# Performance work log

Measured on AMD Instinct MI355X. Metric: run time of the kernel, lower is better.

Reference implementation:

```python
import jax, jax.numpy as jnp
import numpy as np

IMG = 224          # mask height/width, hardcoded in the module
OUT = 256          # Linear(224*224 -> 256)
BOX = 20           # half-width of the square mask around the farthest joint


def setup_inputs() -> dict:
    key = jax.random.key(0)
    k1, k2, k3, k4 = jax.random.split(key, 4)
    B, J, T = 256, 25, 64
    rgbfuture = jax.random.normal(k1, (B, OUT), dtype=jnp.float32)
    # normalized joint coords kept in [0.1, 0.9] so pixel_x in [22, 201] (original
    # code has no x-clamping and would hit numpy negative-slice wraparound otherwise)
    skeleton_future = 0.1 + 0.8 * jax.random.uniform(k2, (B, J, T, 3), dtype=jnp.float32)
    W = jax.random.normal(k3, (OUT, IMG * IMG), dtype=jnp.float32) / np.sqrt(IMG * IMG)
    b = jax.random.normal(k4, (OUT,), dtype=jnp.float32) * 0.01
    return {"rgbfuture": rgbfuture, "skeleton_future": skeleton_future, "W": W, "b": b}


def reference(rgbfuture, skeleton_future, W, b):
    B, J, T, _ = skeleton_future.shape
    mid = J // 2

    # distance of every joint trajectory to the middle joint, per frame: [B, J, T]
    diff = skeleton_future - skeleton_future[:, mid:mid + 1]
    dist = jnp.linalg.norm(diff, axis=-1)
    t_max = jnp.argmax(dist, axis=-1)                       # [B, J]

    # farthest-frame coordinates per joint: [B, J, 3]
    pts = jnp.take_along_axis(skeleton_future, t_max[:, :, None, None], axis=2)[:, :, 0, :]
    px = (pts[..., 0] * IMG).astype(jnp.int32)              # int() truncation == floor (positive)
    py = (pts[..., 1] * IMG).astype(jnp.int32)

    rows = jnp.arange(IMG)
    # x-range: [px-20, px+20) (inputs guarantee in-frame)
    xm = (rows >= (px - BOX)[..., None]) & (rows < (px + BOX)[..., None])   # [B, J, IMG]
    # y-range with the module's explicit edge handling
    y_lo = jnp.where(py < BOX, 0, py - BOX)
    y_hi = jnp.where(py > IMG - BOX, IMG, py + BOX)
    ym = (rows >= y_lo[..., None]) & (rows < y_hi[..., None])               # [B, J, IMG]

    keep = jnp.arange(J) != mid                              # middle joint is skipped
    box = xm[:, :, :, None] & ym[:, :, None, :] & keep[None, :, None, None]  # [B, J, IMG, IMG]
    mask = jnp.any(box, axis=1).astype(rgbfuture.dtype)      # torch.max over joints == union

    merged = mask.reshape(B, IMG * IMG) @ W.T + b            # [B, 256]
    return rgbfuture * merged
```

## Files before the change

### kernel.cpp

```cpp
#include <hip/hip_runtime.h>
#include <hip/hip_bf16.h>
#include <stdint.h>

#define IMG   224
#define OUTD  256
#define BATCH 256
#define JD    25
#define TD    64
#define MIDJ  12
#define BOXR  20

typedef float vfloat4 __attribute__((ext_vector_type(4)));

#define OFF_EV   25804800u
#define OFF_EVC  27901952u
#define OFF_PART 27910144u


__global__ void KA(const float* __restrict__ W, __hip_bfloat16* __restrict__ P,
                   const float* __restrict__ skel, uint32_t* __restrict__ evlist,
                   uint32_t* __restrict__ evcnt) {
    const int id  = blockIdx.x;
    const int tid = threadIdx.x;

    __shared__ float lds[64][225];
    __shared__ float carry[8][64];
    __shared__ int s_px[JD], s_ylo[JD], s_yhi[JD];
    __shared__ uint32_t s_n[IMG];

    if (id < 896) {
        const int xcd = id & 7;
        const int g   = id >> 3;
        const int oc  = g & 3;
        const int xi  = g >> 2;
        const int x   = xcd * 28 + xi;
        const int o0  = oc * 64;

        #pragma unroll
        for (int it = 0; it < 7; ++it) {
            const int k = it * 512 + tid;
            const int r = k / 56;
            const int c = k - r * 56;
            const vfloat4 v = __builtin_nontemporal_load(
                (const vfloat4*)&W[(size_t)(o0 + r) * (IMG * IMG) + (size_t)x * IMG + c * 4]);
            lds[r][c * 4 + 0] = v.x;
            lds[r][c * 4 + 1] = v.y;
            lds[r][c * 4 + 2] = v.z;
            lds[r][c * 4 + 3] = v.w;
        }
        __syncthreads();

        const int ol  = tid & 63;
        const int seg = tid >> 6;
        const int y0  = seg * 28;

        float ssum = 0.0f;
        #pragma unroll
        for (int i = 0; i < 28; ++i) ssum += lds[ol][y0 + i];
        carry[seg][ol] = ssum;
        __syncthreads();

        float s = 0.0f;
        for (int s2 = 0; s2 < seg; ++s2) s += carry[s2][ol];

        __hip_bfloat16* p = P + ((size_t)x * 225) * 256 + o0 + ol;
        if (seg == 0) p[0] = __float2bfloat16(0.0f);
        #pragma unroll
        for (int i = 0; i < 28; ++i) {
            s += lds[ol][y0 + i];
            p[(size_t)(y0 + i + 1) * 256] = __float2bfloat16(s);
        }
        return;
    }

    const int b = id - 896;
    const int wave = tid >> 6;
    const int t = tid & 63;

    const float* sb = skel + (size_t)b * JD * TD * 3;
    const float mx = sb[(MIDJ * TD + t) * 3 + 0];
    const float my = sb[(MIDJ * TD + t) * 3 + 1];
    const float mz = sb[(MIDJ * TD + t) * 3 + 2];

    for (int j = wave; j < JD; j += 8) {
        const float ax = sb[(j * TD + t) * 3 + 0];
        const float ay = sb[(j * TD + t) * 3 + 1];
        const float az = sb[(j * TD + t) * 3 + 2];
        const float dx = ax - mx, dy = ay - my, dz = az - mz;
        const float d2 = __fadd_rn(__fadd_rn(__fmul_rn(dx, dx), __fmul_rn(dy, dy)),
                                   __fmul_rn(dz, dz));
        float bd = sqrtf(d2);
        int   bi = t;
        #pragma unroll
        for (int off = 1; off < 64; off <<= 1) {
            const float od = __shfl_xor(bd, off);
            const int   oi = __shfl_xor(bi, off);
            if (od > bd || (od == bd && oi < bi)) { bd = od; bi = oi; }
        }
        if (t == 0) {
            const float ptx = sb[(j * TD + bi) * 3 + 0];
            const float pty = sb[(j * TD + bi) * 3 + 1];
            const int px = (int)(ptx * 224.0f);
            const int py = (int)(pty * 224.0f);
            s_px[j]  = px;
            s_ylo[j] = (py < BOXR) ? 0 : (py - BOXR);
            s_yhi[j] = (py > IMG - BOXR) ? IMG : (py + BOXR);
        }
    }
    __syncthreads();

    const int x = tid;
    unsigned long long m0 = 0, m1 = 0, m2 = 0, m3 = 0;
    uint32_t n = 0;
    if (x < IMG) {
        for (int j = 0; j < JD; ++j) {
            if (j == MIDJ) continue;
            const int px = s_px[j];
            if (x >= px - BOXR && x < px + BOXR) {
                const int lo = s_ylo[j], hi = s_yhi[j];
                auto setw = [&](unsigned long long& mw, int wbase) {
                    int l = lo - wbase; int h = hi - wbase;
                    l = l < 0 ? 0 : l; h = h > 64 ? 64 : h;
                    if (l < h) {
                        unsigned long long msk =
                            (h - l == 64) ? ~0ull : ((((1ull << (h - l)) - 1ull)) << l);
                        mw |= msk;
                    }
                };
                setw(m0, 0); setw(m1, 64); setw(m2, 128); setw(m3, 192);
            }
        }
        const unsigned long long e0 = m0 & ~(m0 << 1);
        const unsigned long long e1 = m1 & ~((m1 << 1) | (m0 >> 63));
        const unsigned long long e2 = m2 & ~((m2 << 1) | (m1 >> 63));
        const unsigned long long e3 = m3 & ~((m3 << 1) | (m2 >> 63));
        n = (uint32_t)(__popcll(e0) + __popcll(e1) + __popcll(e2) + __popcll(e3));
        s_n[x] = n;
    }
    __syncthreads();
    if (x >= IMG) return;

    const int sl = x / 28;
    const int xl = x - sl * 28;
    uint32_t off = 0;
    for (int i = sl * 28; i < x; ++i) off += s_n[i];
    if (xl == 27) evcnt[(size_t)b * 8 + sl] = off + n;

    uint32_t* evs = evlist + ((size_t)b * 8 + sl) * 256 + off;
    int k = 0, start = -1;
    auto scanw = [&](unsigned long long bits, int wbase) {
        int pos = 0;
        while (pos < 64) {
            if (start < 0) {
                const unsigned long long tt = bits >> pos;
                if (!tt) return;
                pos += __builtin_ctzll(tt);
                start = wbase + pos;
            } else {
                const unsigned long long tt = (~bits) >> pos;
                if (!tt) return;
                pos += __builtin_ctzll(tt);
                evs[k] = (uint32_t)xl | ((uint32_t)start << 5)
                                      | ((uint32_t)(wbase + pos) << 13);
                ++k; start = -1;
            }
        }
    };
    scanw(m0, 0); scanw(m1, 64); scanw(m2, 128); scanw(m3, 192);
    if (start >= 0) { evs[k] = (uint32_t)xl | ((uint32_t)start << 5) | (224u << 13); }
}

__global__ void k_accum(const uint32_t* __restrict__ evlist,
                        const uint32_t* __restrict__ evcnt,
                        const uint32_t* __restrict__ P32,
                        float* __restrict__ part) {
    const int bs  = blockIdx.x;
    const int s   = bs & 7;
    const int tid = threadIdx.x;
    const int x0  = s * 28;

    __shared__ uint32_t slist[256];

    const uint32_t cntv = evcnt[bs];
    slist[tid]       = evlist[(size_t)bs * 256 + tid];
    slist[128 + tid] = evlist[(size_t)bs * 256 + 128 + tid];
    __syncthreads();

    const int total = (int)cntv;
    const uint32_t* Pbase = P32 + (size_t)x0 * (225 * 128) + tid;

    float a0 = 0.f, a1 = 0.f, b0 = 0.f, b1 = 0.f;
    float c0 = 0.f, c1 = 0.f, d0 = 0.f, d1 = 0.f;
    int i = 0;
    for (; i + 4 <= total; i += 4) {
        const uint32_t e0 = slist[i], e1 = slist[i + 1];
        const uint32_t e2 = slist[i + 2], e3 = slist[i + 3];
        const uint32_t* p0 = Pbase + (size_t)(e0 & 31u) * (225 * 128);
        const uint32_t* p1 = Pbase + (size_t)(e1 & 31u) * (225 * 128);
        const uint32_t* p2 = Pbase + (size_t)(e2 & 31u) * (225 * 128);
        const uint32_t* p3 = Pbase + (size_t)(e3 & 31u) * (225 * 128);
        const uint32_t va0 = p0[(size_t)((e0 >> 5) & 255u) * 128];
        const uint32_t vc0 = p0[(size_t)((e0 >> 13) & 255u) * 128];
        const uint32_t va1 = p1[(size_t)((e1 >> 5) & 255u) * 128];
        const uint32_t vc1 = p1[(size_t)((e1 >> 13) & 255u) * 128];
        const uint32_t va2 = p2[(size_t)((e2 >> 5) & 255u) * 128];
        const uint32_t vc2 = p2[(size_t)((e2 >> 13) & 255u) * 128];
        const uint32_t va3 = p3[(size_t)((e3 >> 5) & 255u) * 128];
        const uint32_t vc3 = p3[(size_t)((e3 >> 13) & 255u) * 128];
        a0 += __uint_as_float(vc0 << 16) - __uint_as_float(va0 << 16);
        a1 += __uint_as_float(vc0 & 0xffff0000u) - __uint_as_float(va0 & 0xffff0000u);
        b0 += __uint_as_float(vc1 << 16) - __uint_as_float(va1 << 16);
        b1 += __uint_as_float(vc1 & 0xffff0000u) - __uint_as_float(va1 & 0xffff0000u);
        c0 += __uint_as_float(vc2 << 16) - __uint_as_float(va2 << 16);
        c1 += __uint_as_float(vc2 & 0xffff0000u) - __uint_as_float(va2 & 0xffff0000u);
        d0 += __uint_as_float(vc3 << 16) - __uint_as_float(va3 << 16);
        d1 += __uint_as_float(vc3 & 0xffff0000u) - __uint_as_float(va3 & 0xffff0000u);
    }
    for (; i < total; ++i) {
        const uint32_t e0 = slist[i];
        const uint32_t* p0 = Pbase + (size_t)(e0 & 31u) * (225 * 128);
        const uint32_t va0 = p0[(size_t)((e0 >> 5) & 255u) * 128];
        const uint32_t vc0 = p0[(size_t)((e0 >> 13) & 255u) * 128];
        a0 += __uint_as_float(vc0 << 16) - __uint_as_float(va0 << 16);
        a1 += __uint_as_float(vc0 & 0xffff0000u) - __uint_as_float(va0 & 0xffff0000u);
    }

    float* pp = part + ((size_t)bs * 256) + (size_t)tid * 2;
    pp[0] = (a0 + b0) + (c0 + d0);
    pp[1] = (a1 + b1) + (c1 + d1);
}

__global__ void k_final(const float* __restrict__ rgb, const float* __restrict__ bias,
                        const float* __restrict__ part, float* __restrict__ out) {
    const int idx = blockIdx.x * 256 + threadIdx.x;
    const int b = idx >> 8, o = idx & 255;
    float m = bias[o];
    #pragma unroll
    for (int s = 0; s < 8; ++s) m += part[(((size_t)b * 8 + s) * 256) + o];
    out[idx] = rgb[idx] * m;
}

extern "C" void kernel_launch(void* const* d_in, const int* in_sizes, int n_in,
                              void* d_out, int out_size, void* d_ws, size_t ws_size,
                              hipStream_t stream) {
    const float* rgb  = (const float*)d_in[0];
    const float* skel = (const float*)d_in[1];
    const float* W    = (const float*)d_in[2];
    const float* bias = (const float*)d_in[3];
    float* out = (float*)d_out;

    uint8_t* ws = (uint8_t*)d_ws;
    __hip_bfloat16* P = (__hip_bfloat16*)(ws);
    uint32_t* evlist = (uint32_t*)(ws + OFF_EV);
    uint32_t* evcnt  = (uint32_t*)(ws + OFF_EVC);
    float* part = (float*)(ws + OFF_PART);

    KA<<<dim3(1152), dim3(512), 0, stream>>>(W, P, skel, evlist, evcnt);
    k_accum<<<dim3(BATCH * 8), dim3(128), 0, stream>>>(evlist, evcnt, (const uint32_t*)P, part);
    k_final<<<dim3(BATCH), dim3(256), 0, stream>>>(rgb, bias, part, out);
}
```

Baseline: 41.76 us.

## Split x-range into 16 slices, widen gather unroll, cache prefix row in registers

```diff
diff --git a/kernel.cpp b/kernel.cpp
--- a/kernel.cpp
+++ b/kernel.cpp
@@ -9,12 +9,14 @@
 #define TD    64
 #define MIDJ  12
 #define BOXR  20
+#define NSL   16
+#define SLW   14
 
 typedef float vfloat4 __attribute__((ext_vector_type(4)));
 
 #define OFF_EV   25804800u
-#define OFF_EVC  27901952u
-#define OFF_PART 27910144u
+#define OFF_EVC  29999104u
+#define OFF_PART 30015488u
 
 
 __global__ void KA(const float* __restrict__ W, __hip_bfloat16* __restrict__ P,
@@ -30,23 +32,25 @@
 
     if (id < 896) {
         const int xcd = id & 7;
-        const int g   = id >> 3;
-        const int oc  = g & 3;
-        const int xi  = g >> 2;
-        const int x   = xcd * 28 + xi;
+        const int r   = id >> 3;
+        const int oc  = r & 3;
+        const int q   = r >> 2;
+        const int xi  = q % 14;
+        const int hi8 = q / 14;
+        const int x   = (hi8 * 8 + xcd) * SLW + xi;
         const int o0  = oc * 64;
 
         #pragma unroll
         for (int it = 0; it < 7; ++it) {
             const int k = it * 512 + tid;
-            const int r = k / 56;
-            const int c = k - r * 56;
+            const int rr = k / 56;
+            const int c  = k - rr * 56;
             const vfloat4 v = __builtin_nontemporal_load(
-                (const vfloat4*)&W[(size_t)(o0 + r) * (IMG * IMG) + (size_t)x * IMG + c * 4]);
-            lds[r][c * 4 + 0] = v.x;
-            lds[r][c * 4 + 1] = v.y;
-            lds[r][c * 4 + 2] = v.z;
-            lds[r][c * 4 + 3] = v.w;
+                (const vfloat4*)&W[(size_t)(o0 + rr) * (IMG * IMG) + (size_t)x * IMG + c * 4]);
+            lds[rr][c * 4 + 0] = v.x;
+            lds[rr][c * 4 + 1] = v.y;
+            lds[rr][c * 4 + 2] = v.z;
+            lds[rr][c * 4 + 3] = v.w;
         }
         __syncthreads();
 
@@ -54,9 +58,13 @@
         const int seg = tid >> 6;
         const int y0  = seg * 28;
 
+        float rv[28];
+        #pragma unroll
+        for (int i = 0; i < 28; ++i) rv[i] = lds[ol][y0 + i];
+
         float ssum = 0.0f;
         #pragma unroll
-        for (int i = 0; i < 28; ++i) ssum += lds[ol][y0 + i];
+        for (int i = 0; i < 28; ++i) ssum += rv[i];
         carry[seg][ol] = ssum;
         __syncthreads();
 
@@ -67,7 +75,7 @@
         if (seg == 0) p[0] = __float2bfloat16(0.0f);
         #pragma unroll
         for (int i = 0; i < 28; ++i) {
-            s += lds[ol][y0 + i];
+            s += rv[i];
             p[(size_t)(y0 + i + 1) * 256] = __float2bfloat16(s);
         }
         return;
@@ -140,13 +148,13 @@
     __syncthreads();
     if (x >= IMG) return;
 
-    const int sl = x / 28;
-    const int xl = x - sl * 28;
+    const int sl = x / SLW;
+    const int xl = x - sl * SLW;
     uint32_t off = 0;
-    for (int i = sl * 28; i < x; ++i) off += s_n[i];
-    if (xl == 27) evcnt[(size_t)b * 8 + sl] = off + n;
-
-    uint32_t* evs = evlist + ((size_t)b * 8 + sl) * 256 + off;
+    for (int i = sl * SLW; i < x; ++i) off += s_n[i];
+    if (xl == SLW - 1) evcnt[(size_t)b * NSL + sl] = off + n;
+
+    uint32_t* evs = evlist + ((size_t)b * NSL + sl) * 256 + off;
     int k = 0, start = -1;
     auto scanw = [&](unsigned long long bits, int wbase) {
         int pos = 0;
@@ -175,9 +183,9 @@
                         const uint32_t* __restrict__ P32,
                         float* __restrict__ part) {
     const int bs  = blockIdx.x;
-    const int s   = bs & 7;
+    const int s   = bs & (NSL - 1);
     const int tid = threadIdx.x;
-    const int x0  = s * 28;
+    const int x0  = s * SLW;
 
     __shared__ uint32_t slist[256];
 
@@ -189,45 +197,42 @@
     const int total = (int)cntv;
     const uint32_t* Pbase = P32 + (size_t)x0 * (225 * 128) + tid;
 
-    float a0 = 0.f, a1 = 0.f, b0 = 0.f, b1 = 0.f;
-    float c0 = 0.f, c1 = 0.f, d0 = 0.f, d1 = 0.f;
+    float aLo[8] = {0.f,0.f,0.f,0.f,0.f,0.f,0.f,0.f};
+    float aHi[8] = {0.f,0.f,0.f,0.f,0.f,0.f,0.f,0.f};
     int i = 0;
-    for (; i + 4 <= total; i += 4) {
-        const uint32_t e0 = slist[i], e1 = slist[i + 1];
-        const uint32_t e2 = slist[i + 2], e3 = slist[i + 3];
-        const uint32_t* p0 = Pbase + (size_t)(e0 & 31u) * (225 * 128);
-        const uint32_t* p1 = Pbase + (size_t)(e1 & 31u) * (225 * 128);
-        const uint32_t* p2 = Pbase + (size_t)(e2 & 31u) * (225 * 128);
-        const uint32_t* p3 = Pbase + (size_t)(e3 & 31u) * (225 * 128);
-        const uint32_t va0 = p0[(size_t)((e0 >> 5) & 255u) * 128];
-        const uint32_t vc0 = p0[(size_t)((e0 >> 13) & 255u) * 128];
-        const uint32_t va1 = p1[(size_t)((e1 >> 5) & 255u) * 128];
-        const uint32_t vc1 = p1[(size_t)((e1 >> 13) & 255u) * 128];
-        const uint32_t va2 = p2[(size_t)((e2 >> 5) & 255u) * 128];
-        const uint32_t vc2 = p2[(size_t)((e2 >> 13) & 255u) * 128];
-        const uint32_t va3 = p3[(size_t)((e3 >> 5) & 255u) * 128];
-        const uint32_t vc3 = p3[(size_t)((e3 >> 13) & 255u) * 128];
-        a0 += __uint_as_float(vc0 << 16) - __uint_as_float(va0 << 16);
-        a1 += __uint_as_float(vc0 & 0xffff0000u) - __uint_as_float(va0 & 0xffff0000u);
-        b0 += __uint_as_float(vc1 << 16) - __uint_as_float(va1 << 16);
-        b1 += __uint_as_float(vc1 & 0xffff0000u) - __uint_as_float(va1 & 0xffff0000u);
-        c0 += __uint_as_float(vc2 << 16) - __uint_as_float(va2 << 16);
-        c1 += __uint_as_float(vc2 & 0xffff0000u) - __uint_as_float(va2 & 0xffff0000u);
-        d0 += __uint_as_float(vc3 << 16) - __uint_as_float(va3 << 16);
-        d1 += __uint_as_float(vc3 & 0xffff0000u) - __uint_as_float(va3 & 0xffff0000u);
+    for (; i + 8 <= total; i += 8) {
+        uint32_t ev[8], va[8], vc[8];
+        #pragma unroll
+        for (int u = 0; u < 8; ++u) ev[u] = slist[i + u];
+        #pragma unroll
+        for (int u = 0; u < 8; ++u) {
+            const uint32_t* p = Pbase + (size_t)(ev[u] & 31u) * (225 * 128);
+            va[u] = p[(size_t)((ev[u] >> 5) & 255u) * 128];
+            vc[u] = p[(size_t)((ev[u] >> 13) & 255u) * 128];
+        }
+        #pragma unroll
+        for (int u = 0; u < 8; ++u) {
+            aLo[u] += __uint_as_float(vc[u] << 16) - __uint_as_float(va[u] << 16);
+            aHi[u] += __uint_as_float(vc[u] & 0xffff0000u) - __uint_as_float(va[u] & 0xffff0000u);
+        }
     }
     for (; i < total; ++i) {
         const uint32_t e0 = slist[i];
         const uint32_t* p0 = Pbase + (size_t)(e0 & 31u) * (225 * 128);
         const uint32_t va0 = p0[(size_t)((e0 >> 5) & 255u) * 128];
         const uint32_t vc0 = p0[(size_t)((e0 >> 13) & 255u) * 128];
-        a0 += __uint_as_float(vc0 << 16) - __uint_as_float(va0 << 16);
-        a1 += __uint_as_float(vc0 & 0xffff0000u) - __uint_as_float(va0 & 0xffff0000u);
-    }
+        aLo[0] += __uint_as_float(vc0 << 16) - __uint_as_float(va0 << 16);
+        aHi[0] += __uint_as_float(vc0 & 0xffff0000u) - __uint_as_float(va0 & 0xffff0000u);
+    }
+
+    const float lo = ((aLo[0] + aLo[1]) + (aLo[2] + aLo[3]))
+                   + ((aLo[4] + aLo[5]) + (aLo[6] + aLo[7]));
+    const float hi = ((aHi[0] + aHi[1]) + (aHi[2] + aHi[3]))
+                   + ((aHi[4] + aHi[5]) + (aHi[6] + aHi[7]));
 
     float* pp = part + ((size_t)bs * 256) + (size_t)tid * 2;
-    pp[0] = (a0 + b0) + (c0 + d0);
-    pp[1] = (a1 + b1) + (c1 + d1);
+    pp[0] = lo;
+    pp[1] = hi;
 }
 
 __global__ void k_final(const float* __restrict__ rgb, const float* __restrict__ bias,
@@ -236,7 +241,7 @@
     const int b = idx >> 8, o = idx & 255;
     float m = bias[o];
     #pragma unroll
-    for (int s = 0; s < 8; ++s) m += part[(((size_t)b * 8 + s) * 256) + o];
+    for (int s = 0; s < NSL; ++s) m += part[(((size_t)b * NSL + s) * 256) + o];
     out[idx] = rgb[idx] * m;
 }
 
@@ -256,6 +261,6 @@
     float* part = (float*)(ws + OFF_PART);
 
     KA<<<dim3(1152), dim3(512), 0, stream>>>(W, P, skel, evlist, evcnt);
-    k_accum<<<dim3(BATCH * 8), dim3(128), 0, stream>>>(evlist, evcnt, (const uint32_t*)P, part);
+    k_accum<<<dim3(BATCH * NSL), dim3(128), 0, stream>>>(evlist, evcnt, (const uint32_t*)P, part);
     k_final<<<dim3(BATCH), dim3(256), 0, stream>>>(rgb, bias, part, out);
 }
```

After: 40.10 us. -4.0%, faster.
